# Optimization experiments

Measured on AMD Instinct MI355X. Metric: run time of the kernel, lower is better.

The kernel has to match this reference:

```python
import jax, jax.numpy as jnp
import numpy as np
import math

B, F, NB, H1, H2, K = 16384, 64, 64, 128, 128, 3
LN_EPS = 1e-5


def setup_inputs() -> dict:
    key = jax.random.key(0)
    ks = jax.random.split(key, 16)
    x = jax.random.normal(ks[0], (B, F), dtype=jnp.float32)
    # RBF params (per feature): centers init linspace(-3,3), log_widths = log(step)
    centers = jnp.broadcast_to(jnp.linspace(-3.0, 3.0, NB), (F, NB)).astype(jnp.float32)
    step = 6.0 / (NB - 1)
    log_widths = jnp.full((F, NB), math.log(step), dtype=jnp.float32)
    def lin(k, shape, fan_in):
        return jax.random.normal(k, shape, dtype=jnp.float32) / np.sqrt(fan_in)
    W1 = lin(ks[1], (F, NB, H1), NB); b1 = jnp.zeros((F, H1), jnp.float32)
    g1 = jnp.ones((F, H1), jnp.float32); be1 = jnp.zeros((F, H1), jnp.float32)
    W2 = lin(ks[2], (F, H1, H2), H1); b2 = jnp.zeros((F, H2), jnp.float32)
    g2 = jnp.ones((F, H2), jnp.float32); be2 = jnp.zeros((F, H2), jnp.float32)
    Wr = lin(ks[3], (F, NB, H2), NB); br = jnp.zeros((F, H2), jnp.float32)
    att = jnp.zeros((F,), jnp.float32)
    bias = jnp.zeros((H2,), jnp.float32)
    Wpi = lin(ks[4], (H2, K), H2); bpi = jnp.zeros((K,), jnp.float32)
    Wa = lin(ks[5], (H2, K), H2); ba = jnp.zeros((K,), jnp.float32)
    Wb = lin(ks[6], (H2, K), H2); bb = jnp.zeros((K,), jnp.float32)
    return dict(x=x, centers=centers, log_widths=log_widths, W1=W1, b1=b1, g1=g1,
                be1=be1, W2=W2, b2=b2, g2=g2, be2=be2, Wr=Wr, br=br, att=att,
                bias=bias, Wpi=Wpi, bpi=bpi, Wa=Wa, ba=ba, Wb=Wb, bb=bb)


def _layernorm(h, g, b):
    mu = jnp.mean(h, axis=-1, keepdims=True)
    var = jnp.mean((h - mu) ** 2, axis=-1, keepdims=True)
    return (h - mu) * jax.lax.rsqrt(var + LN_EPS) * g + b


def reference(x, centers, log_widths, W1, b1, g1, be1, W2, b2, g2, be2, Wr, br,
              att, bias, Wpi, bpi, Wa, ba, Wb, bb):
    # RBF expansion, feature axis batched: x [B,F] -> [B,F,NB]
    xc = jnp.clip(x, -10.0, 10.0)
    widths = jnp.exp(jnp.clip(log_widths, -5.0, 5.0)) + 0.1  # [F,NB]
    dist = (xc[:, :, None] - centers[None]) / widths[None]
    rbf = jnp.exp(-0.5 * jnp.clip(dist, -10.0, 10.0) ** 2)  # [B,F,NB]
    # per-feature MLP (grouped GEMMs via einsum)
    h = jnp.einsum('bfn,fnh->bfh', rbf, W1) + b1[None]
    h = jax.nn.gelu(_layernorm(h, g1[None], be1[None]), approximate=False)
    h = jnp.einsum('bfh,fhk->bfk', h, W2) + b2[None]
    h = jax.nn.gelu(_layernorm(h, g2[None], be2[None]), approximate=False)
    res = jnp.einsum('bfn,fnh->bfh', rbf, Wr) + br[None]
    stacked = h + 0.1 * res  # [B,F,H2]
    # attention-weighted aggregation over features
    w = jax.nn.softmax(att)
    agg = jnp.einsum('bfh,f->bh', stacked, w) + bias  # [B,H2]
    # mixture-beta head
    pi = jax.nn.softmax(agg @ Wpi + bpi, axis=-1)
    alpha = jnp.clip(jax.nn.softplus(agg @ Wa + ba) + 1.01, 1.01, 100.0)
    beta = jnp.clip(jax.nn.softplus(agg @ Wb + bb) + 1.01, 1.01, 100.0)
    pred = jnp.sum(pi * (alpha / (alpha + beta)), axis=-1)
    return jnp.clip(pred, 0.001, 0.999)
```

## Files before the change

kernel.cpp:

```cpp
#include <hip/hip_runtime.h>
#include <math.h>

#define BQ   16384
#define FQ   64
#define NBQ  64
#define HD   128
#define FG   4
#define FPG  16
#define MT   128
#define NT   512

typedef __attribute__((ext_vector_type(8))) short s16x8;
typedef __attribute__((ext_vector_type(4))) float f32x4;

__device__ __forceinline__ unsigned short f2bf(float x) {
    unsigned int u = __float_as_uint(x);
    return (unsigned short)((u + 0x7FFFu + ((u >> 16) & 1u)) >> 16);
}
__device__ __forceinline__ unsigned short bftr(float x) {
    return (unsigned short)(__float_as_uint(x) >> 16);
}

__device__ __forceinline__ float softplus_stable(float v) {
    return (v > 0.0f) ? (v + log1pf(expf(-v))) : log1pf(expf(v));
}

__device__ __forceinline__ f32x4 gelu4(f32x4 v) {
    const f32x4 v2 = v * v;
    const f32x4 tt = v2 * (-0.07135481f) + (-1.5957691f);
    const f32x4 s  = v * tt;
    f32x4 r;
    r[0] = __fdividef(v[0], 1.0f + __expf(s[0]));
    r[1] = __fdividef(v[1], 1.0f + __expf(s[1]));
    r[2] = __fdividef(v[2], 1.0f + __expf(s[2]));
    r[3] = __fdividef(v[3], 1.0f + __expf(s[3]));
    return r;
}

__device__ __forceinline__ float dppsum16(float x) {
    int t;
    t = __builtin_amdgcn_update_dpp(0, __float_as_int(x), 0xB1,  0xF, 0xF, true);
    x += __int_as_float(t);
    t = __builtin_amdgcn_update_dpp(0, __float_as_int(x), 0x4E,  0xF, 0xF, true);
    x += __int_as_float(t);
    t = __builtin_amdgcn_update_dpp(0, __float_as_int(x), 0x125, 0xF, 0xF, true);
    x += __int_as_float(t);
    t = __builtin_amdgcn_update_dpp(0, __float_as_int(x), 0x129, 0xF, 0xF, true);
    x += __int_as_float(t);
    return x;
}

__device__ __forceinline__ void load16_lds(const unsigned short* g, unsigned short* l) {
    __builtin_amdgcn_global_load_lds(
        (const __attribute__((address_space(1))) unsigned int*)(uintptr_t)g,
        (__attribute__((address_space(3))) unsigned int*)(uintptr_t)l,
        16, 0, 0);
}

__device__ __forceinline__ int hofs(int row, int col) {
    return row * 128 + (col ^ (((row >> 2) & 3) << 4));
}

__global__ void __launch_bounds__(256) prep_misc(
    const float* __restrict__ att, const float* __restrict__ log_widths,
    const float* __restrict__ centers, const float* __restrict__ br,
    const float* __restrict__ bias,
    const float* __restrict__ b1, const float* __restrict__ g1, const float* __restrict__ be1,
    const float* __restrict__ b2, const float* __restrict__ g2, const float* __restrict__ be2,
    float* __restrict__ wsoft, float* __restrict__ crw2, float* __restrict__ rbias,
    float* __restrict__ Pk)
{
    const int t = threadIdx.x;
    if (blockIdx.x == 0) {
        __shared__ float ws[64];
        if (t < 64) {
            float v = att[t];
            float m = v;
#pragma unroll
            for (int s = 32; s >= 1; s >>= 1) m = fmaxf(m, __shfl_xor(m, s, 64));
            float e = expf(v - m);
            float ssum = e;
#pragma unroll
            for (int s = 32; s >= 1; s >>= 1) ssum += __shfl_xor(ssum, s, 64);
            const float w = e / ssum;
            ws[t] = w;
            wsoft[t] = w;
        }
        __syncthreads();
        for (int i = t; i < FQ * NBQ; i += 256) {
            float lw = fminf(fmaxf(log_widths[i], -5.0f), 5.0f);
            const float rw = 1.0f / (expf(lw) + 0.1f);
            ((float2*)crw2)[i] = make_float2(rw, -centers[i] * rw);
        }
        if (t < HD) {
            float s = bias[t];
            for (int f = 0; f < FQ; ++f) s += 0.1f * ws[f] * br[f * HD + t];
            rbias[t] = s;
        }
    } else {
        const int id = (blockIdx.x - 1) * 256 + t;
        if (id < FQ * HD) {
            ((float4*)Pk)[id * 2]     = make_float4(b1[id], g1[id], be1[id], 0.0f);
            ((float4*)Pk)[id * 2 + 1] = make_float4(b2[id], g2[id], be2[id], 0.0f);
        }
    }
}

__global__ void __launch_bounds__(256) prep_swz(
    const float* __restrict__ W1, const float* __restrict__ Wr, const float* __restrict__ W2,
    unsigned short* __restrict__ W1s, unsigned short* __restrict__ Wrs,
    unsigned short* __restrict__ W2s)
{
    const int gid = blockIdx.x * 256 + threadIdx.x;
    const float* W; unsigned short* dst; int K, id;
    if (gid < 65536)       { W = W1; dst = W1s; K = 64;  id = gid; }
    else if (gid < 131072) { W = Wr; dst = Wrs; K = 64;  id = gid - 65536; }
    else                   { W = W2; dst = W2s; K = 128; id = gid - 131072; }
    const int KB = K >> 3;
    const int nn = id & 15;
    const int kb = (id >> 4) % KB;
    const int nt = ((id >> 4) / KB) & 7;
    const int f  = id / (KB * 16 * 8);
    const float* src = W + ((size_t)f * K + kb * 8) * HD + nt * 16 + nn;
    s16x8 o;
#pragma unroll
    for (int j = 0; j < 8; ++j) o[j] = (short)f2bf(src[(size_t)j * HD]);
    *(s16x8*)(dst + (size_t)f * K * HD + ((size_t)(nt * KB + kb) * 16 + nn) * 8) = o;
}

__global__ void __launch_bounds__(256) prep_xtr(const float* __restrict__ x,
                                                float* __restrict__ xT) {
    __shared__ float tile[64][65];
    const int t  = threadIdx.x;
    const int b0 = blockIdx.x * 64;
    {
        const int row = t & 63, cg = (t >> 6) * 16;
        const float4* src = (const float4*)(x + (size_t)(b0 + row) * FQ + cg);
#pragma unroll
        for (int i = 0; i < 4; ++i) {
            const float4 v = src[i];
            tile[row][cg + i * 4 + 0] = v.x;
            tile[row][cg + i * 4 + 1] = v.y;
            tile[row][cg + i * 4 + 2] = v.z;
            tile[row][cg + i * 4 + 3] = v.w;
        }
    }
    __syncthreads();
    {
        const int f = t >> 2, r0 = (t & 3) * 16;
        float* dst = xT + (size_t)f * BQ + b0 + r0;
#pragma unroll
        for (int i = 0; i < 16; ++i) dst[i] = tile[r0 + i][f];
    }
}

__global__ void __launch_bounds__(NT, 4) nam_main(
    const float* __restrict__ crw2,
    const float* __restrict__ xT,
    const unsigned short* __restrict__ W1s,
    const unsigned short* __restrict__ Wrs,
    const unsigned short* __restrict__ W2s,
    const float* __restrict__ Pk,
    const float* __restrict__ wsoft,
    float* __restrict__ agg)
{
    __shared__ __align__(16) unsigned short wbuf[16384];
    __shared__ __align__(16) unsigned short hbuf[16384];

    const int t    = threadIdx.x;
    const int ln   = t & 63;
    const int wv   = t >> 6;
    const int n    = ln & 15;
    const int q    = ln >> 4;
    const int wrow = wv * 16;
    const int fg   = blockIdx.x & 3;
    const int rb   = blockIdx.x >> 2;
    const int b0   = rb * MT;

    f32x4 acc[8];
#pragma unroll
    for (int nt = 0; nt < 8; ++nt) acc[nt] = f32x4{0.f, 0.f, 0.f, 0.f};

    for (int ff = 0; ff < FPG; ++ff) {
        const int f = fg * FPG + ((ff + rb) & (FPG - 1));
        __syncthreads();

        {
            const unsigned short* gw1 = W1s + (size_t)f * 8192;
            const unsigned short* gwr = Wrs + (size_t)f * 8192;
#pragma unroll
            for (int i = 0; i < 4; ++i) {
                const int chunk = i * 8 + wv;
                const unsigned short* src = (chunk < 16) ? (gw1 + chunk * 512)
                                                         : (gwr + (chunk - 16) * 512);
                load16_lds(src + ln * 8, wbuf + chunk * 512);
            }
        }

        s16x8 a0, a1;
        {
            float xv = xT[(size_t)f * BQ + b0 + wrow + n];
            xv = fminf(fmaxf(xv, -10.0f), 10.0f);
            const float4* c4 = ((const float4*)crw2) + f * 32;
            unsigned int p[8];
#pragma unroll
            for (int h = 0; h < 2; ++h) {
#pragma unroll
                for (int i = 0; i < 4; ++i) {
                    const float4 cc = c4[h * 16 + q * 4 + i];
                    const float d0 = fmaf(xv, cc.x, cc.y);
                    const float d1 = fmaf(xv, cc.z, cc.w);
                    const float e0 = __expf(-0.5f * d0 * d0);
                    const float e1 = __expf(-0.5f * d1 * d1);
                    p[h * 4 + i] = __builtin_amdgcn_perm(__float_as_uint(e1),
                                                         __float_as_uint(e0), 0x07060302u);
                }
            }
            int4 pa = make_int4(p[0], p[1], p[2], p[3]);
            int4 pb = make_int4(p[4], p[5], p[6], p[7]);
            a0 = *(s16x8*)&pa;
            a1 = *(s16x8*)&pb;
        }
        const float wf   = wsoft[f];
        const float wf01 = 0.1f * wf;
        __syncthreads();

        f32x4 hc[8];
#pragma unroll
        for (int nt = 0; nt < 8; ++nt) {
            const s16x8 bA = *(const s16x8*)&wbuf[(nt * 8 + 0) * 128 + ln * 8];
            const s16x8 bB = *(const s16x8*)&wbuf[(nt * 8 + 4) * 128 + ln * 8];
            f32x4 z = f32x4{0.f, 0.f, 0.f, 0.f};
            z = __builtin_amdgcn_mfma_f32_16x16x32_bf16(a0, bA, z, 0, 0, 0);
            z = __builtin_amdgcn_mfma_f32_16x16x32_bf16(a1, bB, z, 0, 0, 0);
            hc[nt] = z;
            const s16x8 cA = *(const s16x8*)&wbuf[8192 + (nt * 8 + 0) * 128 + ln * 8];
            const s16x8 cB = *(const s16x8*)&wbuf[8192 + (nt * 8 + 4) * 128 + ln * 8];
            f32x4 y = f32x4{0.f, 0.f, 0.f, 0.f};
            y = __builtin_amdgcn_mfma_f32_16x16x32_bf16(a0, cA, y, 0, 0, 0);
            y = __builtin_amdgcn_mfma_f32_16x16x32_bf16(a1, cB, y, 0, 0, 0);
            acc[nt] = y * wf01 + acc[nt];
        }
        __syncthreads();

        {
            const unsigned short* gw2 = W2s + (size_t)f * 16384;
#pragma unroll
            for (int i = 0; i < 4; ++i) {
                const int chunk = i * 8 + wv;
                load16_lds(gw2 + chunk * 512 + ln * 8, wbuf + chunk * 512);
            }
        }

        const size_t pkb = ((size_t)f * HD + n) * 8;
        f32x4 sm = {0.f, 0.f, 0.f, 0.f}, sq = {0.f, 0.f, 0.f, 0.f};
#pragma unroll
        for (int nt = 0; nt < 8; ++nt) {
            const float4 pA = *(const float4*)(Pk + pkb + nt * 128);
            const f32x4 v = hc[nt] + pA.x;
            hc[nt] = v; sm += v; sq += v * v;
        }
        f32x4 mu4, rs4;
#pragma unroll
        for (int i = 0; i < 4; ++i) {
            const float s  = dppsum16(sm[i]);
            const float qq = dppsum16(sq[i]);
            mu4[i] = s * (1.0f / 128.0f);
            const float var = qq * (1.0f / 128.0f) - mu4[i] * mu4[i];
            rs4[i] = rsqrtf(var + 1e-5f);
        }
#pragma unroll
        for (int nt = 0; nt < 8; ++nt) {
            const float4 pA = *(const float4*)(Pk + pkb + nt * 128);
            const f32x4 sg = rs4 * pA.y;
            const f32x4 y  = (hc[nt] - mu4) * sg + pA.z;
            const f32x4 z  = gelu4(y);
#pragma unroll
            for (int i = 0; i < 4; ++i)
                hbuf[hofs(wrow + q * 4 + i, nt * 16 + n)] = bftr(z[i]);
        }
        __syncthreads();

        s16x8 A2[4];
#pragma unroll
        for (int c = 0; c < 4; ++c)
            A2[c] = *(const s16x8*)&hbuf[hofs(wrow + n, c * 32 + q * 8)];
        f32x4 h2[8];
#pragma unroll
        for (int nt = 0; nt < 8; ++nt) {
            f32x4 z = f32x4{0.f, 0.f, 0.f, 0.f};
#pragma unroll
            for (int c = 0; c < 4; ++c) {
                const s16x8 bF = *(const s16x8*)&wbuf[(nt * 16 + c * 4) * 128 + ln * 8];
                z = __builtin_amdgcn_mfma_f32_16x16x32_bf16(A2[c], bF, z, 0, 0, 0);
            }
            h2[nt] = z;
        }

        sm = f32x4{0.f, 0.f, 0.f, 0.f}; sq = f32x4{0.f, 0.f, 0.f, 0.f};
#pragma unroll
        for (int nt = 0; nt < 8; ++nt) {
            const float4 pB = *(const float4*)(Pk + pkb + nt * 128 + 4);
            const f32x4 v = h2[nt] + pB.x;
            h2[nt] = v; sm += v; sq += v * v;
        }
#pragma unroll
        for (int i = 0; i < 4; ++i) {
            const float s  = dppsum16(sm[i]);
            const float qq = dppsum16(sq[i]);
            mu4[i] = s * (1.0f / 128.0f);
            const float var = qq * (1.0f / 128.0f) - mu4[i] * mu4[i];
            rs4[i] = rsqrtf(var + 1e-5f);
        }
#pragma unroll
        for (int nt = 0; nt < 8; ++nt) {
            const float4 pB = *(const float4*)(Pk + pkb + nt * 128 + 4);
            const f32x4 sg = rs4 * pB.y;
            const f32x4 y  = (h2[nt] - mu4) * sg + pB.z;
            acc[nt] = gelu4(y) * wf + acc[nt];
        }
    }

    float* ap = agg + (size_t)(b0 + wrow + q * 4) * HD + n;
#pragma unroll
    for (int nt = 0; nt < 8; ++nt) {
#pragma unroll
        for (int i = 0; i < 4; ++i) {
            atomicAdd(ap + (size_t)i * HD + nt * 16, acc[nt][i]);
        }
    }
}

__global__ void __launch_bounds__(256) nam_head(
    const float* __restrict__ agg, const float* __restrict__ rbias,
    const float* __restrict__ Wpi, const float* __restrict__ bpi,
    const float* __restrict__ Wa,  const float* __restrict__ ba,
    const float* __restrict__ Wb,  const float* __restrict__ bb,
    float* __restrict__ out)
{
    const int gid  = blockIdx.x * blockDim.x + threadIdx.x;
    const int row  = gid >> 6;
    const int lane = threadIdx.x & 63;
    if (row >= BQ) return;

    const float2 p  = ((const float2*)(agg + (size_t)row * HD))[lane];
    const float2 rb = ((const float2*)rbias)[lane];
    const float ax = p.x + rb.x;
    const float ay = p.y + rb.y;

    const float2* wp = (const float2*)Wpi;
    const float2* wa = (const float2*)Wa;
    const float2* wb = (const float2*)Wb;
    const float2 p01 = wp[lane * 3], p23 = wp[lane * 3 + 1], p45 = wp[lane * 3 + 2];
    const float2 a01 = wa[lane * 3], a23 = wa[lane * 3 + 1], a45 = wa[lane * 3 + 2];
    const float2 b01 = wb[lane * 3], b23 = wb[lane * 3 + 1], b45 = wb[lane * 3 + 2];

    float ppi0 = ax * p01.x + ay * p23.y;
    float ppi1 = ax * p01.y + ay * p45.x;
    float ppi2 = ax * p23.x + ay * p45.y;
    float pa0  = ax * a01.x + ay * a23.y;
    float pa1  = ax * a01.y + ay * a45.x;
    float pa2  = ax * a23.x + ay * a45.y;
    float pb0  = ax * b01.x + ay * b23.y;
    float pb1  = ax * b01.y + ay * b45.x;
    float pb2  = ax * b23.x + ay * b45.y;

#pragma unroll
    for (int s = 32; s >= 1; s >>= 1) {
        ppi0 += __shfl_xor(ppi0, s, 64);
        ppi1 += __shfl_xor(ppi1, s, 64);
        ppi2 += __shfl_xor(ppi2, s, 64);
        pa0  += __shfl_xor(pa0,  s, 64);
        pa1  += __shfl_xor(pa1,  s, 64);
        pa2  += __shfl_xor(pa2,  s, 64);
        pb0  += __shfl_xor(pb0,  s, 64);
        pb1  += __shfl_xor(pb1,  s, 64);
        pb2  += __shfl_xor(pb2,  s, 64);
    }

    if (lane == 0) {
        const float z0 = ppi0 + bpi[0], z1 = ppi1 + bpi[1], z2 = ppi2 + bpi[2];
        const float mz = fmaxf(z0, fmaxf(z1, z2));
        const float e0 = expf(z0 - mz), e1 = expf(z1 - mz), e2 = expf(z2 - mz);
        const float es = e0 + e1 + e2;

        const float al0 = fminf(fmaxf(softplus_stable(pa0 + ba[0]) + 1.01f, 1.01f), 100.0f);
        const float al1 = fminf(fmaxf(softplus_stable(pa1 + ba[1]) + 1.01f, 1.01f), 100.0f);
        const float al2 = fminf(fmaxf(softplus_stable(pa2 + ba[2]) + 1.01f, 1.01f), 100.0f);
        const float bt0 = fminf(fmaxf(softplus_stable(pb0 + bb[0]) + 1.01f, 1.01f), 100.0f);
        const float bt1 = fminf(fmaxf(softplus_stable(pb1 + bb[1]) + 1.01f, 1.01f), 100.0f);
        const float bt2 = fminf(fmaxf(softplus_stable(pb2 + bb[2]) + 1.01f, 1.01f), 100.0f);

        const float pred = (e0 * (al0 / (al0 + bt0))
                          + e1 * (al1 / (al1 + bt1))
                          + e2 * (al2 / (al2 + bt2))) / es;
        out[row] = fminf(fmaxf(pred, 0.001f), 0.999f);
    }
}

extern "C" void kernel_launch(void* const* d_in, const int* in_sizes, int n_in,
                              void* d_out, int out_size, void* d_ws, size_t ws_size,
                              hipStream_t stream) {
    const float* x          = (const float*)d_in[0];
    const float* centers    = (const float*)d_in[1];
    const float* log_widths = (const float*)d_in[2];
    const float* W1   = (const float*)d_in[3];
    const float* b1   = (const float*)d_in[4];
    const float* g1   = (const float*)d_in[5];
    const float* be1  = (const float*)d_in[6];
    const float* W2   = (const float*)d_in[7];
    const float* b2   = (const float*)d_in[8];
    const float* g2   = (const float*)d_in[9];
    const float* be2  = (const float*)d_in[10];
    const float* Wr   = (const float*)d_in[11];
    const float* br   = (const float*)d_in[12];
    const float* att  = (const float*)d_in[13];
    const float* bias = (const float*)d_in[14];
    const float* Wpi  = (const float*)d_in[15];
    const float* bpi  = (const float*)d_in[16];
    const float* Wa   = (const float*)d_in[17];
    const float* ba   = (const float*)d_in[18];
    const float* Wb   = (const float*)d_in[19];
    const float* bb   = (const float*)d_in[20];

    char* ws = (char*)d_ws;
    float*          wsoft = (float*)(ws + 0);
    float*          rbias = (float*)(ws + 1024);
    float*          crw2  = (float*)(ws + 8192);
    float*          Pk    = (float*)(ws + 65536);
    float*          xT    = (float*)(ws + 327680);
    unsigned short* W1s   = (unsigned short*)(ws + 4521984);
    unsigned short* Wrs   = (unsigned short*)(ws + 5570560);
    unsigned short* W2s   = (unsigned short*)(ws + 6619136);
    float*          agg   = (float*)(ws + 8716288);

    prep_misc<<<33, 256, 0, stream>>>(att, log_widths, centers, br, bias,
                                      b1, g1, be1, b2, g2, be2,
                                      wsoft, crw2, rbias, Pk);
    prep_swz<<<1024, 256, 0, stream>>>(W1, Wr, W2, W1s, Wrs, W2s);
    prep_xtr<<<256, 256, 0, stream>>>(x, xT);
    hipMemsetAsync(agg, 0, (size_t)BQ * HD * sizeof(float), stream);

    nam_main<<<(BQ / MT) * FG, NT, 0, stream>>>(crw2, xT, W1s, Wrs, W2s, Pk,
                                                wsoft, agg);

    nam_head<<<BQ / 4, 256, 0, stream>>>(agg, rbias, Wpi, bpi, Wa, ba, Wb, bb,
                                         (float*)d_out);
}
```

Before: 434.2 us.

## Merge prep kernels, register-prefetch weights, replace atomics with partial buffers

The three prep kernels are merged into one launch, and the memset and atomic accumulation are replaced by per-feature-group partial outputs that the head kernel sums. In the main kernel, next-feature W1/Wr weights are now prefetched into registers during compute and written to LDS at the start of the next iteration, instead of async global-to-LDS loads behind a barrier. The LayerNorm affine is also refactored to use fewer ops. This trims launch overhead and atomic traffic and hides weight-load latency, at the cost of more registers (possible occupancy loss), a larger partial buffer and extra reads in the head.

```diff
diff --git a/kernel.cpp b/kernel.cpp
--- a/kernel.cpp
+++ b/kernel.cpp
@@ -61,17 +61,62 @@
     return row * 128 + (col ^ (((row >> 2) & 3) << 4));
 }
 
-__global__ void __launch_bounds__(256) prep_misc(
+__global__ void __launch_bounds__(256) prep_all(
+    const float* __restrict__ x,
     const float* __restrict__ att, const float* __restrict__ log_widths,
     const float* __restrict__ centers, const float* __restrict__ br,
     const float* __restrict__ bias,
+    const float* __restrict__ W1, const float* __restrict__ Wr, const float* __restrict__ W2,
     const float* __restrict__ b1, const float* __restrict__ g1, const float* __restrict__ be1,
     const float* __restrict__ b2, const float* __restrict__ g2, const float* __restrict__ be2,
+    unsigned short* __restrict__ W1s, unsigned short* __restrict__ Wrs,
+    unsigned short* __restrict__ W2s,
+    float* __restrict__ xT,
     float* __restrict__ wsoft, float* __restrict__ crw2, float* __restrict__ rbias,
     float* __restrict__ Pk)
 {
-    const int t = threadIdx.x;
-    if (blockIdx.x == 0) {
+    const int bid = blockIdx.x;
+    const int t   = threadIdx.x;
+
+    if (bid < 1024) {
+        const int gid = bid * 256 + t;
+        const float* W; unsigned short* dst; int K, id;
+        if (gid < 65536)       { W = W1; dst = W1s; K = 64;  id = gid; }
+        else if (gid < 131072) { W = Wr; dst = Wrs; K = 64;  id = gid - 65536; }
+        else                   { W = W2; dst = W2s; K = 128; id = gid - 131072; }
+        const int KB = K >> 3;
+        const int nn = id & 15;
+        const int kb = (id >> 4) % KB;
+        const int nt = ((id >> 4) / KB) & 7;
+        const int f  = id / (KB * 16 * 8);
+        const float* src = W + ((size_t)f * K + kb * 8) * HD + nt * 16 + nn;
+        s16x8 o;
+#pragma unroll
+        for (int j = 0; j < 8; ++j) o[j] = (short)f2bf(src[(size_t)j * HD]);
+        *(s16x8*)(dst + (size_t)f * K * HD + ((size_t)(nt * KB + kb) * 16 + nn) * 8) = o;
+    } else if (bid < 1280) {
+        __shared__ float tile[64][65];
+        const int b0 = (bid - 1024) * 64;
+        {
+            const int row = t & 63, cg = (t >> 6) * 16;
+            const float4* src = (const float4*)(x + (size_t)(b0 + row) * FQ + cg);
+#pragma unroll
+            for (int i = 0; i < 4; ++i) {
+                const float4 v = src[i];
+                tile[row][cg + i * 4 + 0] = v.x;
+                tile[row][cg + i * 4 + 1] = v.y;
+                tile[row][cg + i * 4 + 2] = v.z;
+                tile[row][cg + i * 4 + 3] = v.w;
+            }
+        }
+        __syncthreads();
+        {
+            const int f = t >> 2, r0 = (t & 3) * 16;
+            float* dst = xT + (size_t)f * BQ + b0 + r0;
+#pragma unroll
+            for (int i = 0; i < 16; ++i) dst[i] = tile[r0 + i][f];
+        }
+    } else if (bid == 1280) {
         __shared__ float ws[64];
         if (t < 64) {
             float v = att[t];
@@ -98,59 +143,11 @@
             rbias[t] = s;
         }
     } else {
-        const int id = (blockIdx.x - 1) * 256 + t;
+        const int id = (bid - 1281) * 256 + t;
         if (id < FQ * HD) {
             ((float4*)Pk)[id * 2]     = make_float4(b1[id], g1[id], be1[id], 0.0f);
             ((float4*)Pk)[id * 2 + 1] = make_float4(b2[id], g2[id], be2[id], 0.0f);
         }
-    }
-}
-
-__global__ void __launch_bounds__(256) prep_swz(
-    const float* __restrict__ W1, const float* __restrict__ Wr, const float* __restrict__ W2,
-    unsigned short* __restrict__ W1s, unsigned short* __restrict__ Wrs,
-    unsigned short* __restrict__ W2s)
-{
-    const int gid = blockIdx.x * 256 + threadIdx.x;
-    const float* W; unsigned short* dst; int K, id;
-    if (gid < 65536)       { W = W1; dst = W1s; K = 64;  id = gid; }
-    else if (gid < 131072) { W = Wr; dst = Wrs; K = 64;  id = gid - 65536; }
-    else                   { W = W2; dst = W2s; K = 128; id = gid - 131072; }
-    const int KB = K >> 3;
-    const int nn = id & 15;
-    const int kb = (id >> 4) % KB;
-    const int nt = ((id >> 4) / KB) & 7;
-    const int f  = id / (KB * 16 * 8);
-    const float* src = W + ((size_t)f * K + kb * 8) * HD + nt * 16 + nn;
-    s16x8 o;
-#pragma unroll
-    for (int j = 0; j < 8; ++j) o[j] = (short)f2bf(src[(size_t)j * HD]);
-    *(s16x8*)(dst + (size_t)f * K * HD + ((size_t)(nt * KB + kb) * 16 + nn) * 8) = o;
-}
-
-__global__ void __launch_bounds__(256) prep_xtr(const float* __restrict__ x,
-                                                float* __restrict__ xT) {
-    __shared__ float tile[64][65];
-    const int t  = threadIdx.x;
-    const int b0 = blockIdx.x * 64;
-    {
-        const int row = t & 63, cg = (t >> 6) * 16;
-        const float4* src = (const float4*)(x + (size_t)(b0 + row) * FQ + cg);
-#pragma unroll
-        for (int i = 0; i < 4; ++i) {
-            const float4 v = src[i];
-            tile[row][cg + i * 4 + 0] = v.x;
-            tile[row][cg + i * 4 + 1] = v.y;
-            tile[row][cg + i * 4 + 2] = v.z;
-            tile[row][cg + i * 4 + 3] = v.w;
-        }
-    }
-    __syncthreads();
-    {
-        const int f = t >> 2, r0 = (t & 3) * 16;
-        float* dst = xT + (size_t)f * BQ + b0 + r0;
-#pragma unroll
-        for (int i = 0; i < 16; ++i) dst[i] = tile[r0 + i][f];
     }
 }
 
@@ -162,7 +159,7 @@
     const unsigned short* __restrict__ W2s,
     const float* __restrict__ Pk,
     const float* __restrict__ wsoft,
-    float* __restrict__ agg)
+    float* __restrict__ aggP)
 {
     __shared__ __align__(16) unsigned short wbuf[16384];
     __shared__ __align__(16) unsigned short hbuf[16384];
@@ -181,20 +178,29 @@
 #pragma unroll
     for (int nt = 0; nt < 8; ++nt) acc[nt] = f32x4{0.f, 0.f, 0.f, 0.f};
 
+    {
+        const int f0 = fg * FPG + (rb & (FPG - 1));
+        const unsigned short* gw1 = W1s + (size_t)f0 * 8192;
+        const unsigned short* gwr = Wrs + (size_t)f0 * 8192;
+#pragma unroll
+        for (int i = 0; i < 4; ++i) {
+            const int chunk = i * 8 + wv;
+            const unsigned short* src = (chunk < 16) ? (gw1 + chunk * 512)
+                                                     : (gwr + (chunk - 16) * 512);
+            load16_lds(src + ln * 8, wbuf + chunk * 512);
+        }
+    }
+
+    int4 pf0, pf1, pf2, pf3;
+
     for (int ff = 0; ff < FPG; ++ff) {
         const int f = fg * FPG + ((ff + rb) & (FPG - 1));
-        __syncthreads();
-
-        {
-            const unsigned short* gw1 = W1s + (size_t)f * 8192;
-            const unsigned short* gwr = Wrs + (size_t)f * 8192;
-#pragma unroll
-            for (int i = 0; i < 4; ++i) {
-                const int chunk = i * 8 + wv;
-                const unsigned short* src = (chunk < 16) ? (gw1 + chunk * 512)
-                                                         : (gwr + (chunk - 16) * 512);
-                load16_lds(src + ln * 8, wbuf + chunk * 512);
-            }
+
+        if (ff > 0) {
+            *(int4*)&wbuf[t * 8]         = pf0;
+            *(int4*)&wbuf[4096 + t * 8]  = pf1;
+            *(int4*)&wbuf[8192 + t * 8]  = pf2;
+            *(int4*)&wbuf[12288 + t * 8] = pf3;
         }
 
         s16x8 a0, a1;
@@ -225,6 +231,16 @@
         const float wf01 = 0.1f * wf;
         __syncthreads();
 
+        {
+            const int f2 = fg * FPG + ((ff + 1 + rb) & (FPG - 1));
+            const unsigned short* g1p = W1s + (size_t)f2 * 8192 + t * 8;
+            const unsigned short* grp = Wrs + (size_t)f2 * 8192 + t * 8;
+            pf0 = *(const int4*)(g1p);
+            pf1 = *(const int4*)(g1p + 4096);
+            pf2 = *(const int4*)(grp);
+            pf3 = *(const int4*)(grp + 4096);
+        }
+
         f32x4 hc[8];
 #pragma unroll
         for (int nt = 0; nt < 8; ++nt) {
@@ -273,8 +289,8 @@
         for (int nt = 0; nt < 8; ++nt) {
             const float4 pA = *(const float4*)(Pk + pkb + nt * 128);
             const f32x4 sg = rs4 * pA.y;
-            const f32x4 y  = (hc[nt] - mu4) * sg + pA.z;
-            const f32x4 z  = gelu4(y);
+            const f32x4 c1 = -mu4 * sg + pA.z;
+            const f32x4 z  = gelu4(hc[nt] * sg + c1);
 #pragma unroll
             for (int i = 0; i < 4; ++i)
                 hbuf[hofs(wrow + q * 4 + i, nt * 16 + n)] = bftr(z[i]);
@@ -285,7 +301,6 @@
 #pragma unroll
         for (int c = 0; c < 4; ++c)
             A2[c] = *(const s16x8*)&hbuf[hofs(wrow + n, c * 32 + q * 8)];
-        f32x4 h2[8];
 #pragma unroll
         for (int nt = 0; nt < 8; ++nt) {
             f32x4 z = f32x4{0.f, 0.f, 0.f, 0.f};
@@ -294,15 +309,15 @@
                 const s16x8 bF = *(const s16x8*)&wbuf[(nt * 16 + c * 4) * 128 + ln * 8];
                 z = __builtin_amdgcn_mfma_f32_16x16x32_bf16(A2[c], bF, z, 0, 0, 0);
             }
-            h2[nt] = z;
+            hc[nt] = z;
         }
 
         sm = f32x4{0.f, 0.f, 0.f, 0.f}; sq = f32x4{0.f, 0.f, 0.f, 0.f};
 #pragma unroll
         for (int nt = 0; nt < 8; ++nt) {
             const float4 pB = *(const float4*)(Pk + pkb + nt * 128 + 4);
-            const f32x4 v = h2[nt] + pB.x;
-            h2[nt] = v; sm += v; sq += v * v;
+            const f32x4 v = hc[nt] + pB.x;
+            hc[nt] = v; sm += v; sq += v * v;
         }
 #pragma unroll
         for (int i = 0; i < 4; ++i) {
@@ -316,23 +331,24 @@
         for (int nt = 0; nt < 8; ++nt) {
             const float4 pB = *(const float4*)(Pk + pkb + nt * 128 + 4);
             const f32x4 sg = rs4 * pB.y;
-            const f32x4 y  = (h2[nt] - mu4) * sg + pB.z;
-            acc[nt] = gelu4(y) * wf + acc[nt];
-        }
-    }
-
-    float* ap = agg + (size_t)(b0 + wrow + q * 4) * HD + n;
+            const f32x4 c1 = -mu4 * sg + pB.z;
+            acc[nt] = gelu4(hc[nt] * sg + c1) * wf + acc[nt];
+        }
+        __syncthreads();
+    }
+
+    float* ap = aggP + ((size_t)fg * BQ + b0 + wrow + q * 4) * HD + n;
 #pragma unroll
     for (int nt = 0; nt < 8; ++nt) {
 #pragma unroll
         for (int i = 0; i < 4; ++i) {
-            atomicAdd(ap + (size_t)i * HD + nt * 16, acc[nt][i]);
+            ap[(size_t)i * HD + nt * 16] = acc[nt][i];
         }
     }
 }
 
 __global__ void __launch_bounds__(256) nam_head(
-    const float* __restrict__ agg, const float* __restrict__ rbias,
+    const float* __restrict__ aggP, const float* __restrict__ rbias,
     const float* __restrict__ Wpi, const float* __restrict__ bpi,
     const float* __restrict__ Wa,  const float* __restrict__ ba,
     const float* __restrict__ Wb,  const float* __restrict__ bb,
@@ -343,10 +359,13 @@
     const int lane = threadIdx.x & 63;
     if (row >= BQ) return;
 
-    const float2 p  = ((const float2*)(agg + (size_t)row * HD))[lane];
+    const float2 p0 = ((const float2*)(aggP + (size_t)row * HD))[lane];
+    const float2 p1 = ((const float2*)(aggP + ((size_t)BQ + row) * HD))[lane];
+    const float2 p2 = ((const float2*)(aggP + ((size_t)2 * BQ + row) * HD))[lane];
+    const float2 p3 = ((const float2*)(aggP + ((size_t)3 * BQ + row) * HD))[lane];
     const float2 rb = ((const float2*)rbias)[lane];
-    const float ax = p.x + rb.x;
-    const float ay = p.y + rb.y;
+    const float ax = p0.x + p1.x + p2.x + p3.x + rb.x;
+    const float ay = p0.y + p1.y + p2.y + p3.y + rb.y;
 
     const float2* wp = (const float2*)Wpi;
     const float2* wa = (const float2*)Wa;
@@ -432,18 +451,15 @@
     unsigned short* W1s   = (unsigned short*)(ws + 4521984);
     unsigned short* Wrs   = (unsigned short*)(ws + 5570560);
     unsigned short* W2s   = (unsigned short*)(ws + 6619136);
-    float*          agg   = (float*)(ws + 8716288);
-
-    prep_misc<<<33, 256, 0, stream>>>(att, log_widths, centers, br, bias,
-                                      b1, g1, be1, b2, g2, be2,
-                                      wsoft, crw2, rbias, Pk);
-    prep_swz<<<1024, 256, 0, stream>>>(W1, Wr, W2, W1s, Wrs, W2s);
-    prep_xtr<<<256, 256, 0, stream>>>(x, xT);
-    hipMemsetAsync(agg, 0, (size_t)BQ * HD * sizeof(float), stream);
+    float*          aggP  = (float*)(ws + 8716288);
+
+    prep_all<<<1313, 256, 0, stream>>>(x, att, log_widths, centers, br, bias,
+                                       W1, Wr, W2, b1, g1, be1, b2, g2, be2,
+                                       W1s, Wrs, W2s, xT, wsoft, crw2, rbias, Pk);
 
     nam_main<<<(BQ / MT) * FG, NT, 0, stream>>>(crw2, xT, W1s, Wrs, W2s, Pk,
-                                                wsoft, agg);
-
-    nam_head<<<BQ / 4, 256, 0, stream>>>(agg, rbias, Wpi, bpi, Wa, ba, Wb, bb,
+                                                wsoft, aggP);
+
+    nam_head<<<BQ / 4, 256, 0, stream>>>(aggP, rbias, Wpi, bpi, Wa, ba, Wb, bb,
                                          (float*)d_out);
 }
```

Result: slower. 464.7 us (+7.0%).
